# Optimization experiments

Hardware: AMD Instinct MI355X
Metric: run time of the kernel (lower is better)

Reference implementation:

```python
import jax, jax.numpy as jnp
import numpy as np

NUM_NET = 5
N = 10000        # nodes per net
E = 160000       # edges per net
B = 512          # molecule graphs per batch
FXD = 62         # node feature dim
FXT = 954        # cell feature dim
D = 128          # output_dim
H1 = 10          # heads in first GATConv


def setup_inputs() -> dict:
    key = jax.random.key(0)
    ks = iter(jax.random.split(key, 64))
    f32 = jnp.float32
    p = lambda shape, scale=0.05: jax.random.normal(next(ks), shape, dtype=f32) * scale
    inp = {}
    inp['x1'] = jax.random.normal(next(ks), (NUM_NET, N, FXD), dtype=f32)
    inp['ei1'] = jax.random.randint(next(ks), (NUM_NET, 2, E), 0, N, dtype=jnp.int32)
    b = ((jnp.arange(N) * B) // N).astype(jnp.int32)  # sorted, no empty graphs
    inp['batch1'] = jnp.broadcast_to(b, (NUM_NET, N))
    inp['x2'] = jax.random.normal(next(ks), (NUM_NET, N, FXD), dtype=f32)
    inp['ei2'] = jax.random.randint(next(ks), (NUM_NET, 2, E), 0, N, dtype=jnp.int32)
    inp['batch2'] = jnp.broadcast_to(b, (NUM_NET, N))
    inp['cell'] = jax.random.normal(next(ks), (B, FXT), dtype=f32)
    # per-net GAT params (stacked over NUM_NET)
    inp['W1'] = p((NUM_NET, H1 * D, FXD))
    inp['a1s'] = p((NUM_NET, H1, D)); inp['a1d'] = p((NUM_NET, H1, D))
    inp['b1'] = p((NUM_NET, H1 * D))
    inp['W2'] = p((NUM_NET, D, H1 * D))
    inp['a2s'] = p((NUM_NET, 1, D)); inp['a2d'] = p((NUM_NET, 1, D))
    inp['b2'] = p((NUM_NET, D))
    inp['Wg'] = p((NUM_NET, D, D)); inp['bg'] = p((NUM_NET, D))
    # cell reduction MLP 954->2048->512->256
    inp['Wr1'] = p((2048, FXT)); inp['br1'] = p((2048,))
    inp['Wr2'] = p((512, 2048)); inp['br2'] = p((512,))
    inp['Wr3'] = p((2 * D, 512)); inp['br3'] = p((2 * D,))
    # head MLP 512->2048->512->128->2
    inp['Wf1'] = p((2048, 4 * D)); inp['bf1'] = p((2048,))
    inp['Wf2'] = p((512, 2048)); inp['bf2'] = p((512,))
    inp['Wf3'] = p((128, 512)); inp['bf3'] = p((128,))
    inp['Wo'] = p((2, 128)); inp['bo'] = p((2,))
    return inp


def _gat(x, src, dst, W, a_s, a_d, b):
    # PyG GATConv (eval): linear -> per-head attention logits -> segment softmax over dst -> scatter-sum
    n = x.shape[0]
    H, C = a_s.shape
    h = (x @ W.T).reshape(n, H, C)
    al = (h * a_s).sum(-1)   # [n, H] source term
    ar = (h * a_d).sum(-1)   # [n, H] dest term
    e = jax.nn.leaky_relu(al[src] + ar[dst], negative_slope=0.2)  # [Ee, H]
    m = jax.ops.segment_max(e, dst, num_segments=n)               # self-loops -> no empty segments
    pe = jnp.exp(e - m[dst])
    s = jax.ops.segment_sum(pe, dst, num_segments=n)
    alpha = pe / s[dst]
    out = jax.ops.segment_sum(h[src] * alpha[:, :, None], dst, num_segments=n)
    return out.reshape(n, H * C) + b


def _branch(x, ei, batch, W1, a1s, a1d, b1, W2, a2s, a2d, b2, Wg, bg):
    n = x.shape[0]
    loops = jnp.arange(n, dtype=ei.dtype)  # add_self_loops=True in PyG GATConv
    src = jnp.concatenate([ei[0], loops])
    dst = jnp.concatenate([ei[1], loops])
    h = jax.nn.elu(_gat(x, src, dst, W1, a1s, a1d, b1))
    h = jax.nn.elu(_gat(h, src, dst, W2, a2s, a2d, b2))
    g = jax.ops.segment_max(h, batch, num_segments=B)  # global max pool
    return jax.nn.relu(g @ Wg.T + bg)


def _l2n(v):
    return v / jnp.clip(jnp.linalg.norm(v, axis=1, keepdims=True), 1e-12)


def reference(x1, ei1, batch1, x2, ei2, batch2, cell,
              W1, a1s, a1d, b1, W2, a2s, a2d, b2, Wg, bg,
              Wr1, br1, Wr2, br2, Wr3, br3,
              Wf1, bf1, Wf2, bf2, Wf3, bf3, Wo, bo):
    x11 = jnp.zeros((B, D), dtype=x1.dtype)
    x22 = jnp.zeros((B, D), dtype=x2.dtype)
    for i in range(NUM_NET):
        pr = (W1[i], a1s[i], a1d[i], b1[i], W2[i], a2s[i], a2d[i], b2[i], Wg[i], bg[i])
        x11 = x11 + _branch(x1[i], ei1[i], batch1[i], *pr) / NUM_NET
        x22 = x22 + _branch(x2[i], ei2[i], batch2[i], *pr) / NUM_NET
    c = _l2n(cell)
    c = jax.nn.relu(c @ Wr1.T + br1)
    c = jax.nn.relu(c @ Wr2.T + br2)
    c = jax.nn.relu(c @ Wr3.T + br3)
    xc = _l2n(jnp.concatenate([x11, x22, c], axis=1))
    xc = jax.nn.relu(xc @ Wf1.T + bf1)
    xc = jax.nn.relu(xc @ Wf2.T + bf2)
    xc = jax.nn.relu(xc @ Wf3.T + bf3)
    return xc @ Wo.T + bo
```

## Files before the change

### kernel.cpp

```cpp
#include <hip/hip_runtime.h>
#include <hip/hip_bf16.h>
#include <math.h>

#define NUM_NET 5
#define NN 10000
#define NE 160000
#define BB 512
#define FXD 62
#define FXT 954
#define MP 10112

typedef __bf16 bf16x8 __attribute__((ext_vector_type(8)));
typedef float f32x4 __attribute__((ext_vector_type(4)));
typedef __hip_bfloat16 bf16;

__device__ __forceinline__ float ldf(const void* p, size_t i) {
  return ((const float*)p)[i];
}
__device__ __forceinline__ float lky(float v) { return v > 0.f ? v : 0.2f * v; }
__device__ __forceinline__ float eluf(float v) { return v > 0.f ? v : (__expf(v) - 1.f); }

struct ConvDesc {
  const void* src;
  bf16* dst;
  int M, K, Mp, Kp, mult, add, batch, pad;
};
struct ConvTable { ConvDesc d[11]; };

__global__ void convert_all_kernel(ConvTable tab) {
  ConvDesc c = tab.d[blockIdx.z];
  int b = blockIdx.y;
  if (b >= c.batch) return;
  int wave = threadIdx.x >> 6, lane = threadIdx.x & 63;
  int r = blockIdx.x * 4 + wave;
  if (r >= c.Mp) return;
  const float* srow = (const float*)c.src + ((size_t)b * c.M + r) * c.K;
  bf16* drow = c.dst + (((size_t)(b * c.mult + c.add)) * c.Mp + r) * c.Kp;
  bool rowok = r < c.M;
  for (int k = lane; k < c.Kp; k += 64) {
    float v = (rowok && k < c.K) ? srow[k] : 0.f;
    drow[k] = __float2bfloat16(v);
  }
}

__global__ void hist_kernel(const int* __restrict__ ei1, const int* __restrict__ ei2,
                            int* __restrict__ counts) {
  int z = blockIdx.z;
  int br = z & 1, net = z >> 1;
  const int* base = (br ? ei2 : ei1) + (size_t)net * 2 * NE;
  const int* dst = base + NE;
  int* cnt = counts + (size_t)z * NN;
  int i = blockIdx.x * 256 + threadIdx.x;
  if (i < NE) atomicAdd(&cnt[dst[i]], 1);
}

__global__ void scan_kernel(const int* __restrict__ counts, int* __restrict__ offs) {
  int z = blockIdx.x;
  counts += (size_t)z * NN;
  offs += (size_t)z * (NN + 1);
  __shared__ int sdata[256];
  __shared__ int s_carry;
  int t = threadIdx.x;
  if (t == 0) { s_carry = 0; offs[0] = 0; }
  __syncthreads();
  for (int base = 0; base < NN; base += 1024) {
    int loc = base + t * 4;
    int v[4];
#pragma unroll
    for (int j = 0; j < 4; j++) v[j] = (loc + j < NN) ? counts[loc + j] : 0;
    int sum4 = v[0] + v[1] + v[2] + v[3];
    sdata[t] = sum4;
    __syncthreads();
    for (int o = 1; o < 256; o <<= 1) {
      int x = (t >= o) ? sdata[t - o] : 0;
      __syncthreads();
      sdata[t] += x;
      __syncthreads();
    }
    int running = sdata[t] - sum4 + s_carry;
#pragma unroll
    for (int j = 0; j < 4; j++) {
      running += v[j];
      if (loc + j < NN) offs[loc + j + 1] = running;
    }
    int tot = sdata[255];
    __syncthreads();
    if (t == 0) s_carry += tot;
    __syncthreads();
  }
}

__global__ void scatter_kernel(const int* __restrict__ ei1, const int* __restrict__ ei2,
                               const int* __restrict__ offs, int* __restrict__ fill,
                               int* __restrict__ csrc) {
  int z = blockIdx.z;
  int br = z & 1, net = z >> 1;
  const int* base = (br ? ei2 : ei1) + (size_t)net * 2 * NE;
  const int* src = base;
  const int* dst = base + NE;
  const int* offz = offs + (size_t)z * (NN + 1);
  int* fillz = fill + (size_t)z * NN;
  int* out = csrc + (size_t)z * NE;
  int i = blockIdx.x * 256 + threadIdx.x;
  if (i < NE) {
    int d = dst[i];
    int p = offz[d] + atomicAdd(&fillz[d], 1);
    out[p] = src[i];
  }
}

__global__ __launch_bounds__(256) void walr_kernel(const void* __restrict__ W1,
                                                   const void* __restrict__ a1s,
                                                   const void* __restrict__ a1d,
                                                   bf16* __restrict__ walrb) {
  int net = blockIdx.x / 10, head = blockIdx.x % 10;
  int t = threadIdx.x, w = t >> 6, k = t & 63;
  __shared__ float ps[8][64];
  float accs = 0.f, accd = 0.f;
  for (int c = w; c < 128; c += 4) {
    float wv = (k < FXD)
        ? ldf(W1, (size_t)net * 1280 * FXD + (size_t)(head * 128 + c) * FXD + k) : 0.f;
    float vs = ldf(a1s, (size_t)net * 1280 + head * 128 + c);
    float vd = ldf(a1d, (size_t)net * 1280 + head * 128 + c);
    accs = fmaf(wv, vs, accs);
    accd = fmaf(wv, vd, accd);
  }
  ps[w][k] = accs;
  ps[4 + w][k] = accd;
  __syncthreads();
  if (w == 0) {
    float s = ps[0][k] + ps[1][k] + ps[2][k] + ps[3][k];
    float dd = ps[4][k] + ps[5][k] + ps[6][k] + ps[7][k];
    walrb[(size_t)net * 4096 + head * 64 + k] = __float2bfloat16(s);
    walrb[(size_t)net * 4096 + (16 + head) * 64 + k] = __float2bfloat16(dd);
  }
}

__global__ __launch_bounds__(256) void xagg_kernel(
    const bf16* __restrict__ xpadA, const float* __restrict__ alrA,
    const int* __restrict__ offsA, const int* __restrict__ srcsA,
    bf16* __restrict__ xagg2, int planeBase) {
  int z = blockIdx.z;
  int plane = planeBase + z;
  bf16* xagg = xagg2 + (size_t)z * 10 * MP * 64;
  int d = blockIdx.x, t = threadIdx.x;
  int hA = t >> 5, p = t & 31;
  if (d >= NN) {
    __hip_bfloat162 zz;
    zz.x = __float2bfloat16(0.f);
    zz.y = zz.x;
    ((__hip_bfloat162*)xagg)[((size_t)hA * MP + d) * 32 + p] = zz;
    if (t < 64) ((__hip_bfloat162*)xagg)[((size_t)(8 + hA) * MP + d) * 32 + p] = zz;
    return;
  }
  const __hip_bfloat162* xp2 =
      (const __hip_bfloat162*)(xpadA + (size_t)plane * MP * 64);
  const float* alr = alrA + (size_t)plane * MP * 32;
  const int* offs = offsA + (size_t)plane * (NN + 1);
  const int* srcs = srcsA + (size_t)plane * NE;
  int e0 = offs[d], ne = offs[d + 1] - e0;
  __shared__ float pm[25][10], psh[25][10];
  __shared__ float s_m[10], s_s[10];
  __shared__ float s_alpha[32][10];
  __shared__ int s_src[32];
  __shared__ __hip_bfloat162 s_x[32][32];
  if (t < 250) {
    int grp = t / 10, hh = t - grp * 10;
    float ard = alr[(size_t)d * 32 + 16 + hh];
    float m = -1e30f, s = 0.f;
    if (grp == 0) { m = lky(alr[(size_t)d * 32 + hh] + ard); s = 1.f; }
    for (int i = grp; i < ne; i += 25) {
      int sc = srcs[e0 + i];
      float v = lky(alr[(size_t)sc * 32 + hh] + ard);
      if (v > m) { s = s * __expf(m - v) + 1.f; m = v; }
      else s += __expf(v - m);
    }
    pm[grp][hh] = m; psh[grp][hh] = s;
  }
  __syncthreads();
  if (t < 10) {
    float m = -1e30f, s = 0.f;
    for (int g = 0; g < 25; g++) {
      float mg = pm[g][t], sg = psh[g][t];
      if (sg > 0.f) {
        if (mg > m) { s = s * __expf(m - mg) + sg; m = mg; }
        else s += sg * __expf(mg - m);
      }
    }
    s_m[t] = m; s_s[t] = s;
  }
  __syncthreads();
  float ax = 0.f, ay = 0.f, bx = 0.f, by = 0.f;
  int total = ne + 1;
  for (int c0 = 0; c0 < total; c0 += 32) {
    int cnt = min(32, total - c0);
    if (t < 32) {
      int idx = c0 + t;
      s_src[t] = (idx < ne) ? srcs[e0 + idx] : d;
    }
    __syncthreads();
    for (int i = t; i < cnt * 10; i += 256) {
      int e = i / 10, hh = i - (i / 10) * 10;
      int sc = s_src[e];
      float v = lky(alr[(size_t)sc * 32 + hh] + alr[(size_t)d * 32 + 16 + hh]);
      s_alpha[e][hh] = __expf(v - s_m[hh]) / s_s[hh];
    }
    for (int i = t; i < cnt * 32; i += 256)
      s_x[i >> 5][i & 31] = xp2[(size_t)s_src[i >> 5] * 32 + (i & 31)];
    __syncthreads();
    for (int i = 0; i < cnt; i++) {
      __hip_bfloat162 v = s_x[i][p];
      float vx = __bfloat162float(v.x), vy = __bfloat162float(v.y);
      float a = s_alpha[i][hA];
      ax = fmaf(vx, a, ax);
      ay = fmaf(vy, a, ay);
      if (t < 64) {
        float b = s_alpha[i][8 + hA];
        bx = fmaf(vx, b, bx);
        by = fmaf(vy, b, by);
      }
    }
    __syncthreads();
  }
  __hip_bfloat162 o;
  o.x = __float2bfloat16(ax);
  o.y = __float2bfloat16(ay);
  ((__hip_bfloat162*)xagg)[((size_t)hA * MP + d) * 32 + p] = o;
  if (t < 64) {
    o.x = __float2bfloat16(bx);
    o.y = __float2bfloat16(by);
    ((__hip_bfloat162*)xagg)[((size_t)(8 + hA) * MP + d) * 32 + p] = o;
  }
}

__global__ __launch_bounds__(256) void fused_l1l2_kernel(
    const bf16* __restrict__ xagg2, const bf16* __restrict__ W1b,
    const void* __restrict__ b1raw, const bf16* __restrict__ W2b,
    const void* __restrict__ a2s, const void* __restrict__ a2d,
    float* __restrict__ al2A, float* __restrict__ ar2A,
    bf16* __restrict__ h2all, int planeBase) {
  int zz = blockIdx.z;
  int plane = planeBase + zz;
  int net = plane >> 1;
  long ow1 = (long)net * 1280 * 64;
  long ob1 = (long)net * 1280;
  long ow2 = (long)net * 128 * 1280;
  long oa2 = (long)net * 128;
  const bf16* xagg = xagg2 + (size_t)zz * 10 * MP * 64;
  float* al2p = al2A + (size_t)plane * NN;
  float* ar2p = ar2A + (size_t)plane * NN;
  bf16* h2 = h2all + (size_t)plane * MP * 128;
  int r0 = blockIdx.y * 64;
  __shared__ __align__(16) char uraw[52224];
  bf16* Ah = (bf16*)uraw;
  bf16* W1s = Ah + 64 * 72;
  bf16* Ps = (bf16*)uraw;
  bf16* W2s = Ps + 64 * 136;
  __shared__ float s_dot[2][2][32][2];
  int tid = threadIdx.x, lane = tid & 63, wave = tid >> 6;
  int l15 = lane & 15, quad = lane >> 4;
  int rowHalf = wave >> 1, colHalf = wave & 1;
  int wr = rowHalf * 32, wc = colHalf * 64;
  f32x4 acc2[2][4];
#pragma unroll
  for (int i = 0; i < 2; i++)
#pragma unroll
    for (int j = 0; j < 4; j++) acc2[i][j] = (f32x4){0.f, 0.f, 0.f, 0.f};

  for (int h = 0; h < 10; h++) {
    __syncthreads();
    for (int i = tid; i < 512; i += 256) {
      int r = i >> 3, seg = i & 7;
      *(uint4*)&Ah[r * 72 + seg * 8] =
          *(const uint4*)&xagg[((size_t)h * MP + r0 + r) * 64 + seg * 8];
    }
    for (int i = tid; i < 1024; i += 256) {
      int r = i >> 3, seg = i & 7;
      *(uint4*)&W1s[r * 72 + seg * 8] =
          *(const uint4*)&W1b[ow1 + (size_t)(h * 128 + r) * 64 + seg * 8];
    }
    __syncthreads();
    f32x4 acc1[4][2];
#pragma unroll
    for (int i = 0; i < 4; i++)
#pragma unroll
      for (int j = 0; j < 2; j++) acc1[i][j] = (f32x4){0.f, 0.f, 0.f, 0.f};
#pragma unroll
    for (int kc = 0; kc < 2; kc++) {
      bf16x8 af[4], bfr[2];
#pragma unroll
      for (int mi = 0; mi < 4; mi++)
        af[mi] = *(const bf16x8*)&Ah[(mi * 16 + l15) * 72 + kc * 32 + quad * 8];
#pragma unroll
      for (int ni = 0; ni < 2; ni++)
        bfr[ni] = *(const bf16x8*)&W1s[(wave * 32 + ni * 16 + l15) * 72 + kc * 32 + quad * 8];
#pragma unroll
      for (int mi = 0; mi < 4; mi++)
#pragma unroll
        for (int ni = 0; ni < 2; ni++)
          acc1[mi][ni] = __builtin_amdgcn_mfma_f32_16x16x32_bf16(af[mi], bfr[ni], acc1[mi][ni], 0, 0, 0);
    }
    __syncthreads();
#pragma unroll
    for (int ni = 0; ni < 2; ni++) {
      int pcol = wave * 32 + ni * 16 + l15;
      float bv = ldf(b1raw, ob1 + h * 128 + pcol);
#pragma unroll
      for (int mi = 0; mi < 4; mi++)
#pragma unroll
        for (int r = 0; r < 4; r++)
          Ps[(mi * 16 + quad * 4 + r) * 136 + pcol] =
              __float2bfloat16(eluf(acc1[mi][ni][r] + bv));
    }
    for (int i = tid; i < 2048; i += 256) {
      int r = i >> 4, seg = i & 15;
      *(uint4*)&W2s[r * 136 + seg * 8] =
          *(const uint4*)&W2b[ow2 + (size_t)r * 1280 + h * 128 + seg * 8];
    }
    __syncthreads();
#pragma unroll
    for (int kc = 0; kc < 4; kc++) {
      bf16x8 pa[2], pb[4];
#pragma unroll
      for (int mi = 0; mi < 2; mi++)
        pa[mi] = *(const bf16x8*)&Ps[(wr + mi * 16 + l15) * 136 + kc * 32 + quad * 8];
#pragma unroll
      for (int ni = 0; ni < 4; ni++)
        pb[ni] = *(const bf16x8*)&W2s[(wc + ni * 16 + l15) * 136 + kc * 32 + quad * 8];
#pragma unroll
      for (int mi = 0; mi < 2; mi++)
#pragma unroll
        for (int ni = 0; ni < 4; ni++)
          acc2[mi][ni] = __builtin_amdgcn_mfma_f32_16x16x32_bf16(pa[mi], pb[ni], acc2[mi][ni], 0, 0, 0);
    }
  }
  float asv[4], adv[4];
#pragma unroll
  for (int ni = 0; ni < 4; ni++) {
    int col = wc + ni * 16 + l15;
    asv[ni] = ldf(a2s, oa2 + col);
    adv[ni] = ldf(a2d, oa2 + col);
  }
#pragma unroll
  for (int mi = 0; mi < 2; mi++) {
#pragma unroll
    for (int r = 0; r < 4; r++) {
      int rl = mi * 16 + quad * 4 + r;
      int row = r0 + wr + rl;
      float psum = 0.f, pdum = 0.f;
#pragma unroll
      for (int ni = 0; ni < 4; ni++) {
        float v = acc2[mi][ni][r];
        h2[(size_t)row * 128 + wc + ni * 16 + l15] = __float2bfloat16(v);
        psum = fmaf(v, asv[ni], psum);
        pdum = fmaf(v, adv[ni], pdum);
      }
#pragma unroll
      for (int o = 1; o < 16; o <<= 1) {
        psum += __shfl_xor(psum, o);
        pdum += __shfl_xor(pdum, o);
      }
      if (l15 == 0) {
        s_dot[rowHalf][colHalf][rl][0] = psum;
        s_dot[rowHalf][colHalf][rl][1] = pdum;
      }
    }
  }
  __syncthreads();
  if (tid < 64) {
    int row = r0 + tid;
    if (row < NN) {
      int rh = tid >> 5, rl = tid & 31;
      al2p[row] = s_dot[rh][0][rl][0] + s_dot[rh][1][rl][0];
      ar2p[row] = s_dot[rh][0][rl][1] + s_dot[rh][1][rl][1];
    }
  }
}

__global__ __launch_bounds__(256) void mfma_gemm64(
    const bf16* __restrict__ A, long Az, const bf16* __restrict__ B, long Bz, int bdiv,
    const void* __restrict__ bias, long biasoff, long biaszs,
    float* __restrict__ Cf, long Cfz, int ldcf, int accum, int ncols, int brcol,
    bf16* __restrict__ Cb, long Cbz, int ldcb,
    int K, int act, float scale) {
  int z = blockIdx.z;
  int zb = bdiv ? (z >> 1) : z;
  A += (size_t)z * Az;
  B += (size_t)zb * Bz;
  if (Cf) Cf += (size_t)z * Cfz + (size_t)(z & 1) * brcol;
  if (Cb) Cb += (size_t)z * Cbz;
  const bf16* Ag = A + (size_t)blockIdx.y * 64 * K;
  const bf16* Bg = B + (size_t)blockIdx.x * 64 * K;
  __shared__ __align__(16) bf16 Asm[64 * 40];
  __shared__ __align__(16) bf16 Bsm[64 * 40];
  int tid = threadIdx.x;
  int lane = tid & 63, wave = tid >> 6;
  int wr = (wave >> 1) * 32, wc = (wave & 1) * 32;
  int l15 = lane & 15, quad = lane >> 4;
  f32x4 acc[2][2];
#pragma unroll
  for (int i = 0; i < 2; i++)
#pragma unroll
    for (int j = 0; j < 2; j++) acc[i][j] = (f32x4){0.f, 0.f, 0.f, 0.f};
  int isB = tid >> 7;
  int srow = (tid & 127) >> 1, shalf = tid & 1;
  const bf16* G = isB ? Bg : Ag;
  bf16* S = isB ? Bsm : Asm;
  for (int k0 = 0; k0 < K; k0 += 32) {
    const uint4* g = (const uint4*)(G + (size_t)srow * K + k0 + shalf * 16);
    uint4 v0 = g[0], v1 = g[1];
    __syncthreads();
    *(uint4*)&S[srow * 40 + shalf * 16] = v0;
    *(uint4*)&S[srow * 40 + shalf * 16 + 8] = v1;
    __syncthreads();
    bf16x8 af[2], bfr[2];
#pragma unroll
    for (int mi = 0; mi < 2; mi++)
      af[mi] = *(const bf16x8*)&Asm[(wr + mi * 16 + l15) * 40 + quad * 8];
#pragma unroll
    for (int ni = 0; ni < 2; ni++)
      bfr[ni] = *(const bf16x8*)&Bsm[(wc + ni * 16 + l15) * 40 + quad * 8];
#pragma unroll
    for (int mi = 0; mi < 2; mi++)
#pragma unroll
      for (int ni = 0; ni < 2; ni++)
        acc[mi][ni] = __builtin_amdgcn_mfma_f32_16x16x32_bf16(af[mi], bfr[ni], acc[mi][ni], 0, 0, 0);
  }
#pragma unroll
  for (int ni = 0; ni < 2; ni++) {
    int col = blockIdx.x * 64 + wc + ni * 16 + l15;
    if (col >= ncols) continue;
    float bv = bias ? ldf(bias, biasoff + (size_t)zb * biaszs + col) : 0.f;
#pragma unroll
    for (int mi = 0; mi < 2; mi++) {
      int rbase = blockIdx.y * 64 + wr + mi * 16 + quad * 4;
      f32x4 c = acc[mi][ni];
#pragma unroll
      for (int r = 0; r < 4; r++) {
        float v = c[r] + bv;
        if (act == 1) v = fmaxf(v, 0.f);
        else if (act == 2) v = eluf(v);
        v *= scale;
        if (Cf) {
          size_t ci = (size_t)(rbase + r) * ldcf + col;
          if (accum == 1) Cf[ci] += v;
          else if (accum == 2) atomicAdd(&Cf[ci], v);
          else Cf[ci] = v;
        }
        if (Cb) Cb[(size_t)(rbase + r) * ldcb + col] = __float2bfloat16(v);
      }
    }
  }
}

__global__ __launch_bounds__(256) void gat_agg1_kernel(
    const bf16* __restrict__ h2all, const float* __restrict__ alA, const float* __restrict__ arA,
    const int* __restrict__ offsA, const int* __restrict__ srcsA,
    const void* __restrict__ b2, bf16* __restrict__ out2all) {
  int z = blockIdx.z;
  int net = z >> 1;
  const bf16* h = h2all + (size_t)z * MP * 128;
  const float* al = alA + (size_t)z * NN;
  const float* ar = arA + (size_t)z * NN;
  const int* offs = offsA + (size_t)z * (NN + 1);
  const int* srcs = srcsA + (size_t)z * NE;
  __shared__ float2 s_pair[4][64];
  int wave = threadIdx.x >> 6, lane = threadIdx.x & 63;
  int d = blockIdx.x * 4 + wave;
  if (d >= NN) return;
  int e0 = offs[d], ne = offs[d + 1] - e0;
  int total = ne + 1;
  float ard = ar[d];
  float m, s, vcache = -1e30f;
  if (total <= 64) {
    int sc = (lane < ne) ? srcs[e0 + lane] : d;
    bool act = lane < total;
    vcache = act ? lky(al[sc] + ard) : -1e30f;
    m = vcache;
    s = act ? 1.f : 0.f;
#pragma unroll
    for (int o = 32; o > 0; o >>= 1) {
      float mo = __shfl_xor(m, o), so = __shfl_xor(s, o);
      if (so > 0.f) {
        if (mo > m) { s = s * __expf(m - mo) + so; m = mo; }
        else s += so * __expf(mo - m);
      }
    }
  } else {
    m = -1e30f; s = 0.f;
    for (int idx = lane; idx < total; idx += 64) {
      int sc = (idx < ne) ? srcs[e0 + idx] : d;
      float v = lky(al[sc] + ard);
      if (v > m) { s = s * __expf(m - v) + 1.f; m = v; }
      else s += __expf(v - m);
    }
#pragma unroll
    for (int o = 32; o > 0; o >>= 1) {
      float mo = __shfl_xor(m, o), so = __shfl_xor(s, o);
      if (so > 0.f) {
        if (mo > m) { s = s * __expf(m - mo) + so; m = mo; }
        else s += so * __expf(mo - m);
      }
    }
  }
  float inv_s = 1.f / s;
  float acc0 = 0.f, acc1v = 0.f;
  for (int c0 = 0; c0 < total; c0 += 64) {
    int idx = c0 + lane;
    int cnt = min(64, total - c0);
    if (idx < total) {
      int sc = (idx < ne) ? srcs[e0 + idx] : d;
      float v = (total <= 64) ? vcache : lky(al[sc] + ard);
      float a = __expf(v - m) * inv_s;
      s_pair[wave][lane] = make_float2(__int_as_float(sc), a);
    }
    int i = 0;
    for (; i + 2 <= cnt; i += 2) {
      float2 pA = s_pair[wave][i];
      float2 pB = s_pair[wave][i + 1];
      __hip_bfloat162 vA =
          ((const __hip_bfloat162*)(h + (size_t)__float_as_int(pA.x) * 128))[lane];
      __hip_bfloat162 vB =
          ((const __hip_bfloat162*)(h + (size_t)__float_as_int(pB.x) * 128))[lane];
      acc0 = fmaf(__bfloat162float(vA.x), pA.y, acc0);
      acc1v = fmaf(__bfloat162float(vA.y), pA.y, acc1v);
      acc0 = fmaf(__bfloat162float(vB.x), pB.y, acc0);
      acc1v = fmaf(__bfloat162float(vB.y), pB.y, acc1v);
    }
    if (i < cnt) {
      float2 pA = s_pair[wave][i];
      __hip_bfloat162 vA =
          ((const __hip_bfloat162*)(h + (size_t)__float_as_int(pA.x) * 128))[lane];
      acc0 = fmaf(__bfloat162float(vA.x), pA.y, acc0);
      acc1v = fmaf(__bfloat162float(vA.y), pA.y, acc1v);
    }
  }
  float b0 = ldf(b2, (size_t)net * 128 + 2 * lane);
  float b1v = ldf(b2, (size_t)net * 128 + 2 * lane + 1);
  __hip_bfloat162 o;
  o.x = __float2bfloat16(eluf(acc0 + b0));
  o.y = __float2bfloat16(eluf(acc1v + b1v));
  ((__hip_bfloat162*)(out2all + ((size_t)z * NN + d) * 128))[lane] = o;
}

__global__ __launch_bounds__(256) void pool_max_kernel(const bf16* __restrict__ out2all,
                                                       bf16* __restrict__ gall) {
  int z = blockIdx.z;
  const bf16* h = out2all + (size_t)z * NN * 128;
  bf16* g = gall + (size_t)z * BB * 128;
  int wave = threadIdx.x >> 6, lane = threadIdx.x & 63;
  int b = blockIdx.x * 4 + wave;
  if (b >= BB) return;
  int n0 = (b * NN + BB - 1) / BB;
  int n1 = ((b + 1) * NN + BB - 1) / BB;
  if (n1 > NN) n1 = NN;
  float mx = -1e30f, my = -1e30f;
  for (int n = n0; n < n1; n++) {
    __hip_bfloat162 v = ((const __hip_bfloat162*)(h + (size_t)n * 128))[lane];
    mx = fmaxf(mx, __bfloat162float(v.x));
    my = fmaxf(my, __bfloat162float(v.y));
  }
  __hip_bfloat162 o;
  o.x = __float2bfloat16(mx);
  o.y = __float2bfloat16(my);
  ((__hip_bfloat162*)(g + (size_t)b * 128))[lane] = o;
}

__global__ __launch_bounds__(256) void l2norm_b_kernel(const float* __restrict__ x,
                                                       bf16* __restrict__ y, int Din, int Kp) {
  int r = blockIdx.x, t = threadIdx.x;
  __shared__ float red[256];
  float s = 0.f;
  for (int i = t; i < Din; i += 256) {
    float v = x[(size_t)r * Din + i];
    s += v * v;
  }
  red[t] = s;
  __syncthreads();
  for (int o = 128; o > 0; o >>= 1) { if (t < o) red[t] += red[t + o]; __syncthreads(); }
  float inv = 1.f / fmaxf(sqrtf(red[0]), 1e-12f);
  for (int i = t; i < Kp; i += 256) {
    float v = (i < Din) ? x[(size_t)r * Din + i] : 0.f;
    y[(size_t)r * Kp + i] = __float2bfloat16(v * inv);
  }
}

__global__ void final_out_kernel(const float* __restrict__ f3, const void* __restrict__ Wo,
                                 const void* __restrict__ bo, float* __restrict__ out) {
  int r = blockIdx.x;
  int lane = threadIdx.x;
  float x0 = f3[(size_t)r * 128 + lane], x1v = f3[(size_t)r * 128 + 64 + lane];
  float s0 = x0 * ldf(Wo, lane) + x1v * ldf(Wo, 64 + lane);
  float s1 = x0 * ldf(Wo, 128 + lane) + x1v * ldf(Wo, 192 + lane);
#pragma unroll
  for (int o = 32; o > 0; o >>= 1) { s0 += __shfl_down(s0, o); s1 += __shfl_down(s1, o); }
  if (lane == 0) {
    out[r * 2] = s0 + ldf(bo, 0);
    out[r * 2 + 1] = s1 + ldf(bo, 1);
  }
}


extern "C" void kernel_launch(void* const* d_in, const int* in_sizes, int n_in,
                              void* d_out, int out_size, void* d_ws, size_t ws_size,
                              hipStream_t stream) {
  const void* x1 = d_in[0];
  const int* ei1 = (const int*)d_in[1];
  const void* x2 = d_in[3];
  const int* ei2 = (const int*)d_in[4];
  const void* cell = d_in[6];
  const void* W1 = d_in[7];
  const void* a1s = d_in[8];
  const void* a1d = d_in[9];
  const void* b1 = d_in[10];
  const void* W2 = d_in[11];
  const void* a2s = d_in[12];
  const void* a2d = d_in[13];
  const void* b2 = d_in[14];
  const void* Wg = d_in[15];
  const void* bg = d_in[16];
  const void* Wr1 = d_in[17]; const void* br1 = d_in[18];
  const void* Wr2 = d_in[19]; const void* br2 = d_in[20];
  const void* Wr3 = d_in[21]; const void* br3 = d_in[22];
  const void* Wf1 = d_in[23]; const void* bf1 = d_in[24];
  const void* Wf2 = d_in[25]; const void* bf2 = d_in[26];
  const void* Wf3 = d_in[27]; const void* bf3 = d_in[28];
  const void* Wo = d_in[29]; const void* bo = d_in[30];

  char* base = (char*)d_ws;
  size_t off = 0;
  auto alloc = [&](size_t bytes) -> void* {
    void* p = base + off;
    off = (off + bytes + 255) & ~(size_t)255;
    return p;
  };
  bf16* d_xpad = (bf16*)alloc((size_t)10 * MP * 64 * 2);
  bf16* d_W1b = (bf16*)alloc((size_t)5 * 1280 * 64 * 2);
  bf16* d_W2b = (bf16*)alloc((size_t)5 * 128 * 1280 * 2);
  bf16* d_Wgb = (bf16*)alloc((size_t)5 * 128 * 128 * 2);
  bf16* d_Wr1b = (bf16*)alloc((size_t)2048 * 960 * 2);
  bf16* d_Wr2b = (bf16*)alloc((size_t)512 * 2048 * 2);
  bf16* d_Wr3b = (bf16*)alloc((size_t)256 * 512 * 2);
  bf16* d_Wf1b = (bf16*)alloc((size_t)2048 * 512 * 2);
  bf16* d_Wf2b = (bf16*)alloc((size_t)512 * 2048 * 2);
  bf16* d_Wf3b = (bf16*)alloc((size_t)128 * 512 * 2);
  int* d_offs = (int*)alloc((size_t)10 * (NN + 1) * 4);
  int* d_srcs = (int*)alloc((size_t)10 * NE * 4);
  int* d_cnt = (int*)alloc((size_t)10 * NN * 4);
  bf16* d_walrb = (bf16*)alloc((size_t)5 * 64 * 64 * 2);
  float* d_alr = (float*)alloc((size_t)10 * MP * 32 * 4);
  float* d_al2 = (float*)alloc((size_t)20 * NN * 4);
  float* d_ar2 = d_al2 + (size_t)10 * NN;
  bf16* d_h2all = (bf16*)alloc((size_t)10 * MP * 128 * 2);
  char* uni = base + off;
  size_t avail = (ws_size > off) ? (ws_size - off) : 0;
  size_t need_big = (size_t)10 * 10 * MP * 64 * 2;
  int G = (avail >= need_big + 65536) ? 10 : 2;
  bf16* d_xagg2 = (bf16*)uni;
  bf16* d_out2all = (bf16*)uni;
  bf16* d_gall = (bf16*)(uni + 25600000);
  float* d_xc = (float*)(uni + 26910720);
  bf16* d_xcb = (bf16*)(uni + 27959296);
  bf16* d_cnb = (bf16*)(uni + 28483584);
  bf16* d_m1b = (bf16*)(uni + 29466624);
  bf16* d_m2b = (bf16*)(uni + 31563776);
  float* d_f3 = (float*)(uni + 32088064);

  ConvTable tab;
  tab.d[0] = {x1, d_xpad, NN, FXD, MP, 64, 2, 0, 5, 0};
  tab.d[1] = {x2, d_xpad, NN, FXD, MP, 64, 2, 1, 5, 0};
  tab.d[2] = {W1, d_W1b, 1280, FXD, 1280, 64, 1, 0, 5, 0};
  tab.d[3] = {W2, d_W2b, 128, 1280, 128, 1280, 1, 0, 5, 0};
  tab.d[4] = {Wg, d_Wgb, 128, 128, 128, 128, 1, 0, 5, 0};
  tab.d[5] = {Wr1, d_Wr1b, 2048, FXT, 2048, 960, 1, 0, 1, 0};
  tab.d[6] = {Wr2, d_Wr2b, 512, 2048, 512, 2048, 1, 0, 1, 0};
  tab.d[7] = {Wr3, d_Wr3b, 256, 512, 256, 512, 1, 0, 1, 0};
  tab.d[8] = {Wf1, d_Wf1b, 2048, 512, 2048, 512, 1, 0, 1, 0};
  tab.d[9] = {Wf2, d_Wf2b, 512, 2048, 512, 2048, 1, 0, 1, 0};
  tab.d[10] = {Wf3, d_Wf3b, 128, 512, 128, 512, 1, 0, 1, 0};
  convert_all_kernel<<<dim3((MP + 3) / 4, 5, 11), 256, 0, stream>>>(tab);

  hipMemsetAsync(d_cnt, 0, (size_t)10 * NN * 4, stream);
  hist_kernel<<<dim3((NE + 255) / 256, 1, 10), 256, 0, stream>>>(ei1, ei2, d_cnt);
  scan_kernel<<<10, 256, 0, stream>>>(d_cnt, d_offs);
  hipMemsetAsync(d_cnt, 0, (size_t)10 * NN * 4, stream);
  scatter_kernel<<<dim3((NE + 255) / 256, 1, 10), 256, 0, stream>>>(ei1, ei2, d_offs, d_cnt, d_srcs);

  walr_kernel<<<50, 256, 0, stream>>>(W1, a1s, a1d, d_walrb);
  mfma_gemm64<<<dim3(1, MP / 64, 10), 256, 0, stream>>>(
      d_xpad, (long)MP * 64, d_walrb, 4096, 1, nullptr, 0, 0,
      d_alr, (long)MP * 32, 32, 0, 32, 0, nullptr, 0, 0, 64, 0, 1.f);

  for (int pb = 0; pb < 10; pb += G) {
    xagg_kernel<<<dim3(MP, 1, G), 256, 0, stream>>>(d_xpad, d_alr, d_offs, d_srcs, d_xagg2, pb);
    fused_l1l2_kernel<<<dim3(1, MP / 64, G), 256, 0, stream>>>(
        d_xagg2, d_W1b, b1, d_W2b, a2s, a2d, d_al2, d_ar2, d_h2all, pb);
  }

  hipMemsetAsync(d_xc, 0, (size_t)BB * 512 * 4, stream);
  gat_agg1_kernel<<<dim3(2500, 1, 10), 256, 0, stream>>>(
      d_h2all, d_al2, d_ar2, d_offs, d_srcs, b2, d_out2all);
  pool_max_kernel<<<dim3(BB / 4, 1, 10), 256, 0, stream>>>(d_out2all, d_gall);
  mfma_gemm64<<<dim3(2, BB / 64, 10), 256, 0, stream>>>(
      d_gall, (long)BB * 128, d_Wgb, 128 * 128, 1,
      bg, 0, 128,
      d_xc, 0, 512, 2, 128, 128, nullptr, 0, 0, 128, 1, 0.2f);

  l2norm_b_kernel<<<BB, 256, 0, stream>>>((const float*)cell, d_cnb, FXT, 960);
  mfma_gemm64<<<dim3(32, 8, 1), 256, 0, stream>>>(
      d_cnb, 0, d_Wr1b, 0, 0, br1, 0, 0, nullptr, 0, 0, 0, 1 << 30, 0, d_m1b, 0, 2048, 960, 1, 1.f);
  mfma_gemm64<<<dim3(8, 8, 1), 256, 0, stream>>>(
      d_m1b, 0, d_Wr2b, 0, 0, br2, 0, 0, nullptr, 0, 0, 0, 1 << 30, 0, d_m2b, 0, 512, 2048, 1, 1.f);
  mfma_gemm64<<<dim3(4, 8, 1), 256, 0, stream>>>(
      d_m2b, 0, d_Wr3b, 0, 0, br3, 0, 0, d_xc + 256, 0, 512, 0, 1 << 30, 0, nullptr, 0, 0, 512, 1, 1.f);

  l2norm_b_kernel<<<BB, 256, 0, stream>>>(d_xc, d_xcb, 512, 512);
  mfma_gemm64<<<dim3(32, 8, 1), 256, 0, stream>>>(
      d_xcb, 0, d_Wf1b, 0, 0, bf1, 0, 0, nullptr, 0, 0, 0, 1 << 30, 0, d_m1b, 0, 2048, 512, 1, 1.f);
  mfma_gemm64<<<dim3(8, 8, 1), 256, 0, stream>>>(
      d_m1b, 0, d_Wf2b, 0, 0, bf2, 0, 0, nullptr, 0, 0, 0, 1 << 30, 0, d_m2b, 0, 512, 2048, 1, 1.f);
  mfma_gemm64<<<dim3(2, 8, 1), 256, 0, stream>>>(
      d_m2b, 0, d_Wf3b, 0, 0, bf3, 0, 0, d_f3, 0, 128, 0, 1 << 30, 0, nullptr, 0, 0, 512, 1, 1.f);
  final_out_kernel<<<BB, 64, 0, stream>>>(d_f3, Wo, bo, (float*)d_out);
}
```

Before: 1.075 ms.

## Aggregate 16 destination nodes per block using MFMA over edge-weight matrix

The first-layer attention aggregation now handles 16 destination nodes per block instead of one. Per-node softmax statistics are computed with 16 lanes per node and combined with wave shuffles. The weighted sum over edges is then expressed as a sparse-as-dense bf16 MFMA: a per-chunk attention matrix (heads x 16 dests x 32 edges) times the gathered source features. This cuts block count and scalar FMA loops, and the output is written through a coalesced staged tile. In exchange, attention weights are rounded to bf16 and there is extra zero-fill of the mostly-empty attention matrix for every chunk.

```diff
diff --git a/kernel.cpp b/kernel.cpp
--- a/kernel.cpp
+++ b/kernel.cpp
@@ -143,93 +143,162 @@
   int z = blockIdx.z;
   int plane = planeBase + z;
   bf16* xagg = xagg2 + (size_t)z * 10 * MP * 64;
-  int d = blockIdx.x, t = threadIdx.x;
-  int hA = t >> 5, p = t & 31;
-  if (d >= NN) {
-    __hip_bfloat162 zz;
-    zz.x = __float2bfloat16(0.f);
-    zz.y = zz.x;
-    ((__hip_bfloat162*)xagg)[((size_t)hA * MP + d) * 32 + p] = zz;
-    if (t < 64) ((__hip_bfloat162*)xagg)[((size_t)(8 + hA) * MP + d) * 32 + p] = zz;
+  int d0 = blockIdx.x * 16;
+  int tid = threadIdx.x;
+
+  if (d0 >= NN) {
+    uint4 zz; zz.x = zz.y = zz.z = zz.w = 0u;
+#pragma unroll
+    for (int k = 0; k < 5; k++) {
+      int i = tid + k * 256;
+      int h = i >> 7, rem = i & 127, row = rem >> 3, seg = rem & 7;
+      *(uint4*)&xagg[((size_t)h * MP + d0 + row) * 64 + seg * 8] = zz;
+    }
     return;
   }
-  const __hip_bfloat162* xp2 =
-      (const __hip_bfloat162*)(xpadA + (size_t)plane * MP * 64);
+
+  const bf16* xp = xpadA + (size_t)plane * MP * 64;
   const float* alr = alrA + (size_t)plane * MP * 32;
   const int* offs = offsA + (size_t)plane * (NN + 1);
   const int* srcs = srcsA + (size_t)plane * NE;
-  int e0 = offs[d], ne = offs[d + 1] - e0;
-  __shared__ float pm[25][10], psh[25][10];
-  __shared__ float s_m[10], s_s[10];
-  __shared__ float s_alpha[32][10];
+
+  __shared__ __align__(16) char uraw[23040];
+  bf16* A = (bf16*)uraw;
+  bf16* Xt = A + 6400;
+  bf16* outt = (bf16*)uraw;
+  __shared__ int s_offs[17];
   __shared__ int s_src[32];
-  __shared__ __hip_bfloat162 s_x[32][32];
-  if (t < 250) {
-    int grp = t / 10, hh = t - grp * 10;
-    float ard = alr[(size_t)d * 32 + 16 + hh];
-    float m = -1e30f, s = 0.f;
-    if (grp == 0) { m = lky(alr[(size_t)d * 32 + hh] + ard); s = 1.f; }
-    for (int i = grp; i < ne; i += 25) {
-      int sc = srcs[e0 + i];
-      float v = lky(alr[(size_t)sc * 32 + hh] + ard);
-      if (v > m) { s = s * __expf(m - v) + 1.f; m = v; }
-      else s += __expf(v - m);
-    }
-    pm[grp][hh] = m; psh[grp][hh] = s;
-  }
+  __shared__ int s_dl[32];
+  __shared__ float s_m[16][10], s_sinv[16][10], s_ar[16][10];
+
+  if (tid < 17) s_offs[tid] = offs[d0 + tid];
   __syncthreads();
-  if (t < 10) {
-    float m = -1e30f, s = 0.f;
-    for (int g = 0; g < 25; g++) {
-      float mg = pm[g][t], sg = psh[g][t];
-      if (sg > 0.f) {
-        if (mg > m) { s = s * __expf(m - mg) + sg; m = mg; }
-        else s += sg * __expf(mg - m);
-      }
-    }
-    s_m[t] = m; s_s[t] = s;
-  }
+  int e_begin = s_offs[0];
+  int nreal = s_offs[16] - e_begin;
+  int K_len = nreal + 16;
+
+  {
+    int dl = tid >> 4, par = tid & 15;
+    int d = d0 + dl;
+    float arh[10], mh[10], sh[10];
+#pragma unroll
+    for (int h = 0; h < 10; h++) arh[h] = alr[(size_t)d * 32 + 16 + h];
+#pragma unroll
+    for (int h = 0; h < 10; h++) {
+      if (par == 0) {
+        mh[h] = lky(alr[(size_t)d * 32 + h] + arh[h]);
+        sh[h] = 1.f;
+      } else {
+        mh[h] = -1e30f;
+        sh[h] = 0.f;
+      }
+    }
+    int eb = s_offs[dl], ee = s_offs[dl + 1];
+    for (int e = eb + par; e < ee; e += 16) {
+      int sc = srcs[e];
+      const float* ap = &alr[(size_t)sc * 32];
+#pragma unroll
+      for (int h = 0; h < 10; h++) {
+        float v = lky(ap[h] + arh[h]);
+        if (v > mh[h]) { sh[h] = sh[h] * __expf(mh[h] - v) + 1.f; mh[h] = v; }
+        else sh[h] += __expf(v - mh[h]);
+      }
+    }
+#pragma unroll
+    for (int o = 8; o >= 1; o >>= 1) {
+#pragma unroll
+      for (int h = 0; h < 10; h++) {
+        float mo = __shfl_xor(mh[h], o), so = __shfl_xor(sh[h], o);
+        if (so > 0.f) {
+          if (mo > mh[h]) { sh[h] = sh[h] * __expf(mh[h] - mo) + so; mh[h] = mo; }
+          else sh[h] += so * __expf(mo - mh[h]);
+        }
+      }
+    }
+    if (par == 0) {
+#pragma unroll
+      for (int h = 0; h < 10; h++) {
+        s_m[dl][h] = mh[h];
+        s_sinv[dl][h] = 1.f / sh[h];
+        s_ar[dl][h] = arh[h];
+      }
+    }
+  }
+
+  int lane = tid & 63, wave = tid >> 6;
+  int l15 = lane & 15, quad = lane >> 4;
+  int wc = wave * 16;
+  f32x4 acc[10];
+#pragma unroll
+  for (int h = 0; h < 10; h++) acc[h] = (f32x4){0.f, 0.f, 0.f, 0.f};
+
+  for (int kb = 0; kb < K_len; kb += 32) {
+    int cnt = min(32, K_len - kb);
+    __syncthreads();
+    if (tid < 32) {
+      int sc = d0, dl = -1;
+      if (tid < cnt) {
+        int ke = kb + tid;
+        if (ke < nreal) {
+          int eg = e_begin + ke;
+          sc = srcs[eg];
+          dl = 0;
+#pragma unroll
+          for (int jj = 1; jj < 16; jj++) dl += (eg >= s_offs[jj]);
+        } else {
+          dl = ke - nreal;
+          sc = d0 + dl;
+        }
+      }
+      s_src[tid] = sc;
+      s_dl[tid] = dl;
+    } else {
+      f32x4 zz4 = (f32x4){0.f, 0.f, 0.f, 0.f};
+      for (int i = tid - 32; i < 800; i += 224) ((f32x4*)A)[i] = zz4;
+    }
+    __syncthreads();
+    {
+      int e = tid & 31, fblk = tid >> 5;
+      uint4 v = *(const uint4*)&xp[(size_t)s_src[e] * 64 + fblk * 8];
+      union { uint4 u; short w[8]; } cv;
+      cv.u = v;
+#pragma unroll
+      for (int i = 0; i < 8; i++)
+        ((short*)Xt)[(fblk * 8 + i) * 40 + e] = cv.w[i];
+    }
+    for (int i = tid; i < 320; i += 256) {
+      int e = i & 31, h = i >> 5;
+      int dl = s_dl[e];
+      if (dl >= 0) {
+        int sc = s_src[e];
+        float v = lky(alr[(size_t)sc * 32 + h] + s_ar[dl][h]);
+        float a = __expf(v - s_m[dl][h]) * s_sinv[dl][h];
+        A[(h * 16 + dl) * 40 + e] = __float2bfloat16(a);
+      }
+    }
+    __syncthreads();
+    bf16x8 bfr = *(const bf16x8*)&Xt[(wc + l15) * 40 + quad * 8];
+#pragma unroll
+    for (int h = 0; h < 10; h++) {
+      bf16x8 af = *(const bf16x8*)&A[(h * 16 + l15) * 40 + quad * 8];
+      acc[h] = __builtin_amdgcn_mfma_f32_16x16x32_bf16(af, bfr, acc[h], 0, 0, 0);
+    }
+  }
+
   __syncthreads();
-  float ax = 0.f, ay = 0.f, bx = 0.f, by = 0.f;
-  int total = ne + 1;
-  for (int c0 = 0; c0 < total; c0 += 32) {
-    int cnt = min(32, total - c0);
-    if (t < 32) {
-      int idx = c0 + t;
-      s_src[t] = (idx < ne) ? srcs[e0 + idx] : d;
-    }
-    __syncthreads();
-    for (int i = t; i < cnt * 10; i += 256) {
-      int e = i / 10, hh = i - (i / 10) * 10;
-      int sc = s_src[e];
-      float v = lky(alr[(size_t)sc * 32 + hh] + alr[(size_t)d * 32 + 16 + hh]);
-      s_alpha[e][hh] = __expf(v - s_m[hh]) / s_s[hh];
-    }
-    for (int i = t; i < cnt * 32; i += 256)
-      s_x[i >> 5][i & 31] = xp2[(size_t)s_src[i >> 5] * 32 + (i & 31)];
-    __syncthreads();
-    for (int i = 0; i < cnt; i++) {
-      __hip_bfloat162 v = s_x[i][p];
-      float vx = __bfloat162float(v.x), vy = __bfloat162float(v.y);
-      float a = s_alpha[i][hA];
-      ax = fmaf(vx, a, ax);
-      ay = fmaf(vy, a, ay);
-      if (t < 64) {
-        float b = s_alpha[i][8 + hA];
-        bx = fmaf(vx, b, bx);
-        by = fmaf(vy, b, by);
-      }
-    }
-    __syncthreads();
-  }
-  __hip_bfloat162 o;
-  o.x = __float2bfloat16(ax);
-  o.y = __float2bfloat16(ay);
-  ((__hip_bfloat162*)xagg)[((size_t)hA * MP + d) * 32 + p] = o;
-  if (t < 64) {
-    o.x = __float2bfloat16(bx);
-    o.y = __float2bfloat16(by);
-    ((__hip_bfloat162*)xagg)[((size_t)(8 + hA) * MP + d) * 32 + p] = o;
+#pragma unroll
+  for (int h = 0; h < 10; h++) {
+#pragma unroll
+    for (int r = 0; r < 4; r++)
+      outt[(h * 16 + quad * 4 + r) * 72 + wc + l15] = __float2bfloat16(acc[h][r]);
+  }
+  __syncthreads();
+#pragma unroll
+  for (int k = 0; k < 5; k++) {
+    int i = tid + k * 256;
+    int h = i >> 7, rem = i & 127, row = rem >> 3, seg = rem & 7;
+    uint4 v = *(const uint4*)&outt[(h * 16 + row) * 72 + seg * 8];
+    *(uint4*)&xagg[((size_t)h * MP + d0 + row) * 64 + seg * 8] = v;
   }
 }
 
@@ -692,7 +761,7 @@
       d_alr, (long)MP * 32, 32, 0, 32, 0, nullptr, 0, 0, 64, 0, 1.f);
 
   for (int pb = 0; pb < 10; pb += G) {
-    xagg_kernel<<<dim3(MP, 1, G), 256, 0, stream>>>(d_xpad, d_alr, d_offs, d_srcs, d_xagg2, pb);
+    xagg_kernel<<<dim3(MP / 16, 1, G), 256, 0, stream>>>(d_xpad, d_alr, d_offs, d_srcs, d_xagg2, pb);
     fused_l1l2_kernel<<<dim3(1, MP / 64, G), 256, 0, stream>>>(
         d_xagg2, d_W1b, b1, d_W2b, a2s, a2d, d_al2, d_ar2, d_h2all, pb);
   }
```

Result: faster. 954.8 us (-11.2%).
